# Performance work log

Measured on AMD Instinct MI355X. Metric: run time of the kernel, lower is better.

Reference implementation:

```python
import jax, jax.numpy as jnp
import numpy as np

NUM_HEADS = 12

def setup_inputs() -> dict:
    key = jax.random.key(0)
    k1, k2 = jax.random.split(key)
    X = jax.random.normal(k1, (2, 2048, 768), dtype=jnp.float32)
    # torch nn.Linear(dim, 2*dim, bias=False) weight has shape [2*dim, dim]
    W_qkv = jax.random.normal(k2, (1536, 768), dtype=jnp.float32) * (768 ** -0.5)
    return {"X": X, "W_qkv": W_qkv}

def reference(X, W_qkv):
    B, N, C = X.shape
    H = NUM_HEADS
    hd = C // H
    scale = hd ** -0.5
    # qkv: [B, N, 2, H, hd]
    qkv = (X @ W_qkv.T).reshape(B, N, 2, H, hd)
    q = jnp.transpose(qkv[:, :, 0], (0, 2, 1, 3))  # [B, H, N, hd]
    k = jnp.transpose(qkv[:, :, 1], (0, 2, 1, 3))  # [B, H, N, hd]
    attn = jnp.einsum('bhnd,bhmd->bhnm', q, k) * scale  # [B, H, N, N]
    # dropout p=0 -> identity; double sum over heads and keys
    scores = attn.sum(axis=1).sum(axis=-1)  # [B, N]
    return scores
```

## Files before the change

### kernel.cpp

```cpp
#include <hip/hip_runtime.h>


#define DIM 768
#define SEQ 2048
#define NGRP 16


__global__ void colsum_k(const float* __restrict__ X, float* __restrict__ xpart) {
    int bi = blockIdx.x;
    int b  = bi >> 8;
    int ch = bi & 255;
    int g  = ch >> 4;
    int i  = threadIdx.x;
    const float4* base = (const float4*)(X + ((size_t)b * SEQ + (size_t)ch * 8) * DIM) + i;
    float4 a = {0.f, 0.f, 0.f, 0.f};
    #pragma unroll
    for (int n = 0; n < 8; ++n) {
        float4 x = base[n * 192];
        a.x += x.x; a.y += x.y; a.z += x.z; a.w += x.w;
    }
    float* dst = xpart + (size_t)(b * NGRP + g) * DIM + i * 4;
    atomicAdd(dst + 0, a.x);
    atomicAdd(dst + 1, a.y);
    atomicAdd(dst + 2, a.z);
    atomicAdd(dst + 3, a.w);
}

__global__ void v_k(const float* __restrict__ W, const float* __restrict__ xpart,
                    float* __restrict__ v) {
    __shared__ alignas(16) float xs[DIM];
    int bi   = blockIdx.x;
    int b    = bi / 192;
    int c0   = (bi % 192) * 4;
    int tid  = threadIdx.x;
    int lane = tid & 63;
    int wv   = tid >> 6;

    #pragma unroll
    for (int k = 0; k < 3; ++k) {
        int d = tid + k * 256;
        const float* p = xpart + (size_t)(b * NGRP) * DIM + d;
        float s = 0.f;
        #pragma unroll
        for (int g = 0; g < NGRP; ++g)
            s += p[(size_t)g * DIM];
        xs[d] = s;
    }
    __syncthreads();

    int c = c0 + wv;
    const float4* wr  = (const float4*)(W + (size_t)(DIM + c) * DIM);
    const float4* xs4 = (const float4*)xs;
    float acc = 0.f;
    #pragma unroll
    for (int j = 0; j < 3; ++j) {
        float4 a = wr[lane + 64 * j];
        float4 s = xs4[lane + 64 * j];
        acc += a.x * s.x + a.y * s.y + a.z * s.z + a.w * s.w;
    }
    #pragma unroll
    for (int off = 32; off; off >>= 1) acc += __shfl_down(acc, off, 64);
    if (lane == 0) v[b * DIM + c] = acc;
}

__global__ void t_k(const float* __restrict__ W, const float* __restrict__ v,
                    float* __restrict__ t) {
    int bi  = blockIdx.x;
    int b   = bi / 96;
    int rem = bi % 96;
    int cs  = rem / 3;
    int dch = rem % 3;
    int d   = dch * 256 + threadIdx.x;
    int c0  = cs * 24;
    const float* vb = v + b * DIM;
    float acc = 0.f;
    #pragma unroll 8
    for (int c = c0; c < c0 + 24; ++c)
        acc += W[(size_t)c * DIM + d] * vb[c];
    atomicAdd(&t[b * DIM + d], acc);
}

__global__ void scores_k(const float* __restrict__ X, const float* __restrict__ t,
                         float* __restrict__ out) {
    __shared__ alignas(16) float ft[DIM];
    int bi   = blockIdx.x;
    int b    = bi >> 8;
    int tid  = threadIdx.x;
    int lane = tid & 63;
    int wv   = tid >> 6;

    if (tid < 192)
        ((float4*)ft)[tid] = ((const float4*)(t + b * DIM))[tid];
    __syncthreads();

    const float4* t4 = (const float4*)ft;
    int r0 = bi * 8 + wv * 2;
    #pragma unroll
    for (int rr = 0; rr < 2; ++rr) {
        int r = r0 + rr;
        const float4* xr = (const float4*)(X + (size_t)r * DIM);
        float acc = 0.f;
        #pragma unroll
        for (int j = 0; j < 3; ++j) {
            float4 a = xr[lane + 64 * j];
            float4 s = t4[lane + 64 * j];
            acc += a.x * s.x + a.y * s.y + a.z * s.z + a.w * s.w;
        }
        #pragma unroll
        for (int off = 32; off; off >>= 1) acc += __shfl_down(acc, off, 64);
        if (lane == 0) out[r] = acc * 0.125f;
    }
}

extern "C" void kernel_launch(void* const* d_in, const int* in_sizes, int n_in,
                              void* d_out, int out_size, void* d_ws, size_t ws_size,
                              hipStream_t stream) {
    const float* X = (const float*)d_in[0];
    const float* W = (const float*)d_in[1];
    float* out = (float*)d_out;
    float* ws = (float*)d_ws;
    float* xpart = ws;
    float* v     = ws + 2 * NGRP * DIM;
    float* t     = v + 2 * DIM;

    colsum_k<<<512, 192, 0, stream>>>(X, xpart);
    v_k     <<<384, 256, 0, stream>>>(W, xpart, v);
    t_k     <<<192, 256, 0, stream>>>(W, v, t);
    scores_k<<<512, 256, 0, stream>>>(X, t, out);
}
```

Measured before the change: 76.40 us.

## Fuse four stage kernels into one cooperative kernel with grid syncs

```diff
diff --git a/kernel.cpp b/kernel.cpp
--- a/kernel.cpp
+++ b/kernel.cpp
@@ -1,4 +1,7 @@
 #include <hip/hip_runtime.h>
+#include <hip/hip_cooperative_groups.h>
+
+namespace cg = cooperative_groups;
 
 
 #define DIM 768
@@ -6,109 +9,114 @@
 #define NGRP 16
 
 
-__global__ void colsum_k(const float* __restrict__ X, float* __restrict__ xpart) {
-    int bi = blockIdx.x;
-    int b  = bi >> 8;
-    int ch = bi & 255;
-    int g  = ch >> 4;
-    int i  = threadIdx.x;
-    const float4* base = (const float4*)(X + ((size_t)b * SEQ + (size_t)ch * 8) * DIM) + i;
-    float4 a = {0.f, 0.f, 0.f, 0.f};
-    #pragma unroll
-    for (int n = 0; n < 8; ++n) {
-        float4 x = base[n * 192];
-        a.x += x.x; a.y += x.y; a.z += x.z; a.w += x.w;
+__global__ __launch_bounds__(256, 2)
+void fused_k(const float* __restrict__ X, const float* __restrict__ W,
+             float* __restrict__ out, float* __restrict__ ws) {
+    cg::grid_group grid = cg::this_grid();
+
+    float* xpart = ws;
+    float* v     = ws + 2 * NGRP * DIM;
+    float* t     = v + 2 * DIM;
+
+    __shared__ alignas(16) float sbuf[DIM];
+
+    const int bi   = blockIdx.x;
+    const int tid  = threadIdx.x;
+    const int lane = tid & 63;
+    const int wv   = tid >> 6;
+
+    {
+        int b  = bi >> 8;
+        int ch = bi & 255;
+        int g  = ch >> 4;
+        if (tid < 192) {
+            const float4* base =
+                (const float4*)(X + ((size_t)b * SEQ + (size_t)ch * 8) * DIM) + tid;
+            float4 a = {0.f, 0.f, 0.f, 0.f};
+            #pragma unroll
+            for (int n = 0; n < 8; ++n) {
+                float4 x = base[n * 192];
+                a.x += x.x; a.y += x.y; a.z += x.z; a.w += x.w;
+            }
+            float* dst = xpart + (size_t)(b * NGRP + g) * DIM + tid * 4;
+            atomicAdd(dst + 0, a.x);
+            atomicAdd(dst + 1, a.y);
+            atomicAdd(dst + 2, a.z);
+            atomicAdd(dst + 3, a.w);
+        }
     }
-    float* dst = xpart + (size_t)(b * NGRP + g) * DIM + i * 4;
-    atomicAdd(dst + 0, a.x);
-    atomicAdd(dst + 1, a.y);
-    atomicAdd(dst + 2, a.z);
-    atomicAdd(dst + 3, a.w);
-}
+    grid.sync();
 
-__global__ void v_k(const float* __restrict__ W, const float* __restrict__ xpart,
-                    float* __restrict__ v) {
-    __shared__ alignas(16) float xs[DIM];
-    int bi   = blockIdx.x;
-    int b    = bi / 192;
-    int c0   = (bi % 192) * 4;
-    int tid  = threadIdx.x;
-    int lane = tid & 63;
-    int wv   = tid >> 6;
+    if (bi < 384) {
+        int b  = bi / 192;
+        int c0 = (bi % 192) * 4;
+        #pragma unroll
+        for (int k = 0; k < 3; ++k) {
+            int d = tid + k * 256;
+            const float* p = xpart + (size_t)(b * NGRP) * DIM + d;
+            float s = 0.f;
+            #pragma unroll
+            for (int g = 0; g < NGRP; ++g)
+                s += p[(size_t)g * DIM];
+            sbuf[d] = s;
+        }
+        __syncthreads();
 
-    #pragma unroll
-    for (int k = 0; k < 3; ++k) {
-        int d = tid + k * 256;
-        const float* p = xpart + (size_t)(b * NGRP) * DIM + d;
-        float s = 0.f;
-        #pragma unroll
-        for (int g = 0; g < NGRP; ++g)
-            s += p[(size_t)g * DIM];
-        xs[d] = s;
-    }
-    __syncthreads();
-
-    int c = c0 + wv;
-    const float4* wr  = (const float4*)(W + (size_t)(DIM + c) * DIM);
-    const float4* xs4 = (const float4*)xs;
-    float acc = 0.f;
-    #pragma unroll
-    for (int j = 0; j < 3; ++j) {
-        float4 a = wr[lane + 64 * j];
-        float4 s = xs4[lane + 64 * j];
-        acc += a.x * s.x + a.y * s.y + a.z * s.z + a.w * s.w;
-    }
-    #pragma unroll
-    for (int off = 32; off; off >>= 1) acc += __shfl_down(acc, off, 64);
-    if (lane == 0) v[b * DIM + c] = acc;
-}
-
-__global__ void t_k(const float* __restrict__ W, const float* __restrict__ v,
-                    float* __restrict__ t) {
-    int bi  = blockIdx.x;
-    int b   = bi / 96;
-    int rem = bi % 96;
-    int cs  = rem / 3;
-    int dch = rem % 3;
-    int d   = dch * 256 + threadIdx.x;
-    int c0  = cs * 24;
-    const float* vb = v + b * DIM;
-    float acc = 0.f;
-    #pragma unroll 8
-    for (int c = c0; c < c0 + 24; ++c)
-        acc += W[(size_t)c * DIM + d] * vb[c];
-    atomicAdd(&t[b * DIM + d], acc);
-}
-
-__global__ void scores_k(const float* __restrict__ X, const float* __restrict__ t,
-                         float* __restrict__ out) {
-    __shared__ alignas(16) float ft[DIM];
-    int bi   = blockIdx.x;
-    int b    = bi >> 8;
-    int tid  = threadIdx.x;
-    int lane = tid & 63;
-    int wv   = tid >> 6;
-
-    if (tid < 192)
-        ((float4*)ft)[tid] = ((const float4*)(t + b * DIM))[tid];
-    __syncthreads();
-
-    const float4* t4 = (const float4*)ft;
-    int r0 = bi * 8 + wv * 2;
-    #pragma unroll
-    for (int rr = 0; rr < 2; ++rr) {
-        int r = r0 + rr;
-        const float4* xr = (const float4*)(X + (size_t)r * DIM);
+        int c = c0 + wv;
+        const float4* wr  = (const float4*)(W + (size_t)(DIM + c) * DIM);
+        const float4* xs4 = (const float4*)sbuf;
         float acc = 0.f;
         #pragma unroll
         for (int j = 0; j < 3; ++j) {
-            float4 a = xr[lane + 64 * j];
-            float4 s = t4[lane + 64 * j];
+            float4 a = wr[lane + 64 * j];
+            float4 s = xs4[lane + 64 * j];
             acc += a.x * s.x + a.y * s.y + a.z * s.z + a.w * s.w;
         }
         #pragma unroll
         for (int off = 32; off; off >>= 1) acc += __shfl_down(acc, off, 64);
-        if (lane == 0) out[r] = acc * 0.125f;
+        if (lane == 0) v[b * DIM + c] = acc;
+    }
+    grid.sync();
+
+    if (bi < 192) {
+        int b   = bi / 96;
+        int rem = bi % 96;
+        int cs  = rem / 3;
+        int dch = rem % 3;
+        int d   = dch * 256 + tid;
+        int c0  = cs * 24;
+        const float* vb = v + b * DIM;
+        float acc = 0.f;
+        #pragma unroll 8
+        for (int c = c0; c < c0 + 24; ++c)
+            acc += W[(size_t)c * DIM + d] * vb[c];
+        atomicAdd(&t[b * DIM + d], acc);
+    }
+    grid.sync();
+
+    {
+        int b = bi >> 8;
+        if (tid < 192)
+            ((float4*)sbuf)[tid] = ((const float4*)(t + b * DIM))[tid];
+        __syncthreads();
+
+        const float4* t4 = (const float4*)sbuf;
+        int r0 = bi * 8 + wv * 2;
+        #pragma unroll
+        for (int rr = 0; rr < 2; ++rr) {
+            int r = r0 + rr;
+            const float4* xr = (const float4*)(X + (size_t)r * DIM);
+            float acc = 0.f;
+            #pragma unroll
+            for (int j = 0; j < 3; ++j) {
+                float4 a = xr[lane + 64 * j];
+                float4 s = t4[lane + 64 * j];
+                acc += a.x * s.x + a.y * s.y + a.z * s.z + a.w * s.w;
+            }
+            #pragma unroll
+            for (int off = 32; off; off >>= 1) acc += __shfl_down(acc, off, 64);
+            if (lane == 0) out[r] = acc * 0.125f;
+        }
     }
 }
 
@@ -118,13 +126,9 @@
     const float* X = (const float*)d_in[0];
     const float* W = (const float*)d_in[1];
     float* out = (float*)d_out;
-    float* ws = (float*)d_ws;
-    float* xpart = ws;
-    float* v     = ws + 2 * NGRP * DIM;
-    float* t     = v + 2 * DIM;
+    float* ws  = (float*)d_ws;
 
-    colsum_k<<<512, 192, 0, stream>>>(X, xpart);
-    v_k     <<<384, 256, 0, stream>>>(W, xpart, v);
-    t_k     <<<192, 256, 0, stream>>>(W, v, t);
-    scores_k<<<512, 256, 0, stream>>>(X, t, out);
+    void* args[] = { (void*)&X, (void*)&W, (void*)&out, (void*)&ws };
+    hipLaunchCooperativeKernel(reinterpret_cast<void*>(fused_k),
+                               dim3(512), dim3(256), args, 0, stream);
 }
```

Measured after the change: 254.4 us. 233% more time.
